# Kernel optimization log

Measured on AMD Instinct MI355X. Metric: run time of the kernel, lower is better.

Reference implementation:

```python
import jax, jax.numpy as jnp
import numpy as np

DIM = 192
NUM_HEADS = 6
WH, WW = 7, 7
N = WH * WW  # 49 tokens per window
C2 = 2 * DIM  # concatenated channel dim = 384
SCALE = (DIM // NUM_HEADS) ** -0.5  # module uses dim//num_heads, not C2//num_heads
NW = 64  # number of windows per image
B_ = 2048  # num_windows * batch


def _relative_position_index():
    ch = np.arange(WH)
    cw = np.arange(WW)
    coords = np.stack(np.meshgrid(ch, cw, indexing='ij')).reshape(2, -1)  # [2, N]
    rel = coords[:, :, None] - coords[:, None, :]  # [2, N, N]
    rel = rel.transpose(1, 2, 0).astype(np.int64)  # [N, N, 2]
    rel[..., 0] += WH - 1
    rel[..., 1] += WW - 1
    rel[..., 0] *= 2 * WW - 1
    return jnp.asarray(rel.sum(-1))  # [N, N]

REL_IDX = _relative_position_index()


def setup_inputs() -> dict:
    key = jax.random.key(0)
    ks = jax.random.split(key, 8)
    x = jax.random.normal(ks[0], (B_, N, DIM), dtype=jnp.float32)
    y = jax.random.normal(ks[1], (B_, N, DIM), dtype=jnp.float32)
    mask = jax.random.normal(ks[2], (NW, N, N), dtype=jnp.float32)
    w_qkv = jax.random.normal(ks[3], (6 * DIM, C2), dtype=jnp.float32) * 0.02
    b_qkv = jnp.zeros((6 * DIM,), dtype=jnp.float32)
    w_proj = jax.random.normal(ks[4], (DIM, C2), dtype=jnp.float32) * 0.02
    b_proj = jnp.zeros((DIM,), dtype=jnp.float32)
    bias_table = jax.random.normal(ks[5], ((2 * WH - 1) * (2 * WW - 1), NUM_HEADS), dtype=jnp.float32) * 0.02
    return {"x": x, "y": y, "mask": mask, "w_qkv": w_qkv, "b_qkv": b_qkv,
            "w_proj": w_proj, "b_proj": b_proj, "bias_table": bias_table}


def reference(x, y, mask, w_qkv, b_qkv, w_proj, b_proj, bias_table):
    Bc = x.shape[0]
    Dh = C2 // NUM_HEADS  # 64
    xy = jnp.concatenate([x, y], axis=2)  # [B_, N, 2*dim]
    qkv = xy @ w_qkv.T + b_qkv  # [B_, N, 6*dim]
    qkv = qkv.reshape(Bc, N, 3, NUM_HEADS, Dh).transpose(2, 0, 3, 1, 4)  # [3, B_, H, N, Dh]
    q, k, v = qkv[0] * SCALE, qkv[1], qkv[2]
    attn = jnp.einsum('bhnd,bhmd->bhnm', q, k)  # [B_, H, N, N]
    rpb = bias_table[REL_IDX]  # [N, N, H]
    attn = attn + rpb.transpose(2, 0, 1)[None]
    nW = mask.shape[0]
    attn = attn.reshape(Bc // nW, nW, NUM_HEADS, N, N) + mask[None, :, None]
    attn = attn.reshape(Bc, NUM_HEADS, N, N)
    attn = jax.nn.softmax(attn, axis=-1)
    out = jnp.einsum('bhnm,bhmd->bhnd', attn, v)  # [B_, H, N, Dh]
    out = out.transpose(0, 2, 1, 3).reshape(Bc, N, C2)
    return out @ w_proj.T + b_proj  # [B_, N, dim]
```

## Files before the change

### kernel.cpp

```cpp
#include <hip/hip_runtime.h>
#include <hip/hip_bf16.h>


typedef __attribute__((ext_vector_type(8))) short short8;
typedef __attribute__((ext_vector_type(4))) float f32x4;

#define SCALE 0.17677669529663687f

#define WQF_OFF    0ul
#define WQF_BYTES  (864ul*1024)
#define WPF_OFF    (WQF_OFF + WQF_BYTES)
#define WPF_BYTES  (144ul*1024)
#define COMB_OFF   (WPF_OFF + WPF_BYTES)
#define COMB_BYTES (64ul*6*4096*4)
#define WS_NEED    (COMB_OFF + COMB_BYTES)

__device__ __forceinline__ unsigned short f2bf(float f){
  unsigned u = __builtin_bit_cast(unsigned, f);
  u = u + 0x7fffu + ((u >> 16) & 1u);
  return (unsigned short)(u >> 16);
}
__device__ __forceinline__ unsigned long long pack4(float4 v){
  return (unsigned long long)f2bf(v.x) | ((unsigned long long)f2bf(v.y) << 16)
       | ((unsigned long long)f2bf(v.z) << 32) | ((unsigned long long)f2bf(v.w) << 48);
}

__device__ __forceinline__ unsigned short cvt1(float x){
  unsigned r;
  asm("v_cvt_pk_bf16_f32 %0, %1, %1" : "=v"(r) : "v"(x));
  return (unsigned short)r;
}
__device__ __forceinline__ uint2 pk4(float a, float b, float c, float d){
  unsigned lo, hi;
  asm("v_cvt_pk_bf16_f32 %0, %1, %2" : "=v"(lo) : "v"(a), "v"(b));
  asm("v_cvt_pk_bf16_f32 %0, %1, %2" : "=v"(hi) : "v"(c), "v"(d));
  return make_uint2(lo, hi);
}

__global__ void k_prep(const float* __restrict__ wq_f, const float* __restrict__ wp_f,
                       const float* __restrict__ mask, const float* __restrict__ btab,
                       unsigned short* __restrict__ wqf, unsigned short* __restrict__ wpf,
                       float* __restrict__ comb){
  if (blockIdx.x < 252){
    int t = blockIdx.x*256 + threadIdx.x;
    int fragidx = t >> 6, l = t & 63;
    const float* src; unsigned short* dst;
    float sc = 1.0f;
    if (fragidx < 864){
      int h = fragidx/144, rem = fragidx - h*144;
      int ct = rem/12, kt = rem - ct*12;
      int row = (ct>>2)*384 + h*64 + (ct&3)*16 + (l&15);
      src = wq_f + (long)row*384 + kt*32 + (l>>4)*8;
      dst = wqf + (long)fragidx*512 + l*8;
      if (ct < 4) sc = SCALE;
    } else {
      int fid = fragidx - 864;
      int ct = fid/12, kt = fid - ct*12;
      int row = ct*16 + (l&15);
      src = wp_f + (long)row*384 + kt*32 + (l>>4)*8;
      dst = wpf + (long)fid*512 + l*8;
    }
    short8 v;
    #pragma unroll
    for (int e = 0; e < 8; ++e) v[e] = (short)f2bf(src[e] * sc);
    *(short8*)dst = v;
  } else {
    int idx = (blockIdx.x - 252)*256 + threadIdx.x;
    int j = idx & 63, i = (idx >> 6) & 63, rest = idx >> 12;
    int h = rest % 6, w = rest / 6;
    float v;
    if (i < 49 && j < 49){
      int di = i / 7 - j / 7 + 6;
      int dj = i % 7 - j % 7 + 6;
      v = btab[(di * 13 + dj) * 6 + h] + mask[(w * 49 + i) * 49 + j];
    } else {
      v = (j >= 49) ? -1e30f : 0.0f;
    }
    comb[idx] = v;
  }
}

__device__ __forceinline__ int swz(int r, int b){ return b ^ ((r & 7) << 4); }
__device__ __forceinline__ int a_q (int r, int c){ return 49152 + swz(r, r*128 + c*2); }
__device__ __forceinline__ int a_k (int r, int c){ return 57344 + swz(r, r*128 + c*2); }
__device__ __forceinline__ int a_vt(int r, int c){ return 65536 + swz(r, r*128 + c*2); }
#define OBUF 73728

__global__ __launch_bounds__(256, 2)
void k_fused(const float* __restrict__ x, const float* __restrict__ y,
             const unsigned short* __restrict__ wqf, const unsigned short* __restrict__ wpf,
             const float* __restrict__ bqkv, const float* __restrict__ bproj,
             const float* __restrict__ comb, float* __restrict__ out){
  __shared__ __align__(16) unsigned char smem[81920];
  const int win = blockIdx.x;
  const int tid = threadIdx.x, w = tid>>6, l = tid&63, l15 = l&15, lg = l>>4;

  #pragma unroll
  for (int i = 0; i < 12; ++i){
    int f  = w*12 + i;
    int kt = f >> 2, mt = f & 3;
    int row = mt*16 + l15;
    int c   = kt*32 + lg*8;
    uint4 vv = make_uint4(0,0,0,0);
    if (row < 49){
      const float* src = (c < 192) ? (x + ((long)win*49 + row)*192 + c)
                                   : (y + ((long)win*49 + row)*192 + (c - 192));
      float4 f0 = *(const float4*)src, f1 = *(const float4*)(src + 4);
      uint2 lo = pk4(f0.x, f0.y, f0.z, f0.w);
      uint2 hi = pk4(f1.x, f1.y, f1.z, f1.w);
      vv = make_uint4(lo.x, lo.y, hi.x, hi.y);
    }
    *(uint4*)(smem + f*1024 + l*16) = vv;
  }

  int np[3];
  f32x4 pacc[4][3];
  #pragma unroll
  for (int nt = 0; nt < 3; ++nt){
    np[nt] = w*48 + nt*16 + l15;
    float bv = bproj[np[nt]];
    #pragma unroll
    for (int mt = 0; mt < 4; ++mt)
      #pragma unroll
      for (int j = 0; j < 4; ++j) pacc[mt][nt][j] = bv;
  }

  __syncthreads();

  #pragma unroll 2
  for (int h = 0; h < 6; ++h){
    const float* cb = comb + ((long)((win & 63)*6 + h))*4096 + (w*16 + l15)*64 + lg*4;
    float4 cbv[4];
    #pragma unroll
    for (int nt = 0; nt < 4; ++nt) cbv[nt] = *(const float4*)(cb + nt*16);

    float bias[3];
    #pragma unroll
    for (int nt = 0; nt < 3; ++nt){
      int ct = w*3 + nt, s = ct >> 2;
      bias[nt] = bqkv[s*384 + h*64 + (ct & 3)*16 + l15];
      if (s == 0) bias[nt] *= SCALE;
    }

    const unsigned short* Bb = wqf + ((long)h*12 + w*3)*12*512;
    short8 bB[2][3];
    #pragma unroll
    for (int nt = 0; nt < 3; ++nt)
      bB[0][nt] = *(const short8*)(Bb + (nt*12)*512 + l*8);
    f32x4 acc[4][3];
    #pragma unroll
    for (int mt = 0; mt < 4; ++mt)
      #pragma unroll
      for (int nt = 0; nt < 3; ++nt)
        #pragma unroll
        for (int j = 0; j < 4; ++j) acc[mt][nt][j] = bias[nt];

    #pragma unroll
    for (int kt = 0; kt < 12; ++kt){
      const int cur = kt & 1, nxt = cur ^ 1;
      if (kt < 11){
        #pragma unroll
        for (int nt = 0; nt < 3; ++nt)
          bB[nxt][nt] = *(const short8*)(Bb + (nt*12 + kt+1)*512 + l*8);
      }
      short8 aA[4];
      #pragma unroll
      for (int mt = 0; mt < 4; ++mt)
        aA[mt] = *(const short8*)(smem + (kt*4 + mt)*1024 + l*16);
      __builtin_amdgcn_s_setprio(1);
      #pragma unroll
      for (int nt = 0; nt < 3; ++nt){
        #pragma unroll
        for (int mt = 0; mt < 4; ++mt)
          acc[mt][nt] = __builtin_amdgcn_mfma_f32_16x16x32_bf16(aA[mt], bB[cur][nt], acc[mt][nt], 0, 0, 0);
      }
      __builtin_amdgcn_s_setprio(0);
    }

    #pragma unroll
    for (int nt = 0; nt < 3; ++nt){
      int ct = w*3 + nt, s = ct >> 2, d16 = (ct & 3) * 16;
      if (s == 2){
        #pragma unroll
        for (int mt = 0; mt < 4; ++mt){
          uint2 p = pk4(acc[mt][nt][0], acc[mt][nt][1], acc[mt][nt][2], acc[mt][nt][3]);
          *(uint2*)(smem + a_vt(d16 + l15, mt*16 + lg*4)) = p;
        }
      } else {
        #pragma unroll
        for (int mt = 0; mt < 4; ++mt){
          #pragma unroll
          for (int j = 0; j < 4; ++j){
            int row = mt*16 + lg*4 + j;
            int addr = (s == 0) ? a_q(row, d16 + l15) : a_k(row, d16 + l15);
            *(unsigned short*)(smem + addr) = cvt1(acc[mt][nt][j]);
          }
        }
      }
    }
    __syncthreads();

    short8 bq[2];
    #pragma unroll
    for (int ks = 0; ks < 2; ++ks)
      bq[ks] = *(const short8*)(smem + a_q(w*16 + l15, ks*32 + lg*8));
    f32x4 st[4] = {};
    __builtin_amdgcn_s_setprio(1);
    #pragma unroll
    for (int ks = 0; ks < 2; ++ks){
      #pragma unroll
      for (int nt = 0; nt < 4; ++nt){
        short8 ak = *(const short8*)(smem + a_k(nt*16 + l15, ks*32 + lg*8));
        st[nt] = __builtin_amdgcn_mfma_f32_16x16x32_bf16(ak, bq[ks], st[nt], 0, 0, 0);
      }
    }
    __builtin_amdgcn_s_setprio(0);
    #pragma unroll
    for (int nt = 0; nt < 4; ++nt){
      st[nt][0] += cbv[nt].x; st[nt][1] += cbv[nt].y;
      st[nt][2] += cbv[nt].z; st[nt][3] += cbv[nt].w;
    }
    float mx;
    {
      float m0 = fmaxf(fmaxf(st[0][0], st[0][1]), fmaxf(st[0][2], st[0][3]));
      float m1 = fmaxf(fmaxf(st[1][0], st[1][1]), fmaxf(st[1][2], st[1][3]));
      float m2 = fmaxf(fmaxf(st[2][0], st[2][1]), fmaxf(st[2][2], st[2][3]));
      float m3 = fmaxf(fmaxf(st[3][0], st[3][1]), fmaxf(st[3][2], st[3][3]));
      mx = fmaxf(fmaxf(m0, m1), fmaxf(m2, m3));
    }
    mx = fmaxf(mx, __shfl_xor(mx, 16));
    mx = fmaxf(mx, __shfl_xor(mx, 32));
    float ssum = 0.f;
    #pragma unroll
    for (int nt = 0; nt < 4; ++nt){
      #pragma unroll
      for (int j = 0; j < 4; ++j){
        float e = __expf(st[nt][j] - mx);
        st[nt][j] = e; ssum += e;
      }
    }
    ssum += __shfl_xor(ssum, 16);
    ssum += __shfl_xor(ssum, 32);
    const float inv = 1.0f / ssum;

    #pragma unroll
    for (int nt = 0; nt < 4; ++nt){
      uint2 p = pk4(st[nt][0]*inv, st[nt][1]*inv, st[nt][2]*inv, st[nt][3]*inv);
      *(uint2*)(smem + a_q(w*16 + l15, nt*16 + lg*4)) = p;
    }

    short8 ap[2];
    #pragma unroll
    for (int ks = 0; ks < 2; ++ks)
      ap[ks] = *(const short8*)(smem + a_q(w*16 + l15, ks*32 + lg*8));
    f32x4 oacc[4] = {};
    __builtin_amdgcn_s_setprio(1);
    #pragma unroll
    for (int ks = 0; ks < 2; ++ks){
      #pragma unroll
      for (int nt = 0; nt < 4; ++nt){
        short8 bv = *(const short8*)(smem + a_vt(nt*16 + l15, ks*32 + lg*8));
        oacc[nt] = __builtin_amdgcn_mfma_f32_16x16x32_bf16(ap[ks], bv, oacc[nt], 0, 0, 0);
      }
    }
    __builtin_amdgcn_s_setprio(0);

    short8 pb[2][3];
    #pragma unroll
    for (int ks = 0; ks < 2; ++ks)
      #pragma unroll
      for (int nt = 0; nt < 3; ++nt)
        pb[ks][nt] = *(const short8*)(wpf + ((long)(w*3 + nt)*12 + h*2 + ks)*512 + l*8);

    #pragma unroll
    for (int nt = 0; nt < 4; ++nt){
      int frag  = (nt >> 1)*4 + w;
      int chunk0 = (lg*4) + ((nt & 1)*2 + (l15 >> 3))*16;
      #pragma unroll
      for (int j = 0; j < 4; ++j){
        int addr = OBUF + frag*1024 + (chunk0 + j)*16 + (l15 & 7)*2;
        *(unsigned short*)(smem + addr) = cvt1(oacc[nt][j]);
      }
    }
    __syncthreads();

    #pragma unroll
    for (int ks = 0; ks < 2; ++ks){
      short8 aO[4];
      #pragma unroll
      for (int mt = 0; mt < 4; ++mt)
        aO[mt] = *(const short8*)(smem + OBUF + (ks*4 + mt)*1024 + l*16);
      __builtin_amdgcn_s_setprio(1);
      #pragma unroll
      for (int nt = 0; nt < 3; ++nt){
        #pragma unroll
        for (int mt = 0; mt < 4; ++mt)
          pacc[mt][nt] = __builtin_amdgcn_mfma_f32_16x16x32_bf16(aO[mt], pb[ks][nt], pacc[mt][nt], 0, 0, 0);
      }
      __builtin_amdgcn_s_setprio(0);
    }
  }

  #pragma unroll
  for (int mt = 0; mt < 4; ++mt){
    #pragma unroll
    for (int j = 0; j < 4; ++j){
      int row = mt*16 + lg*4 + j;
      if (row < 49){
        float* o = out + ((long)win*49 + row)*192;
        #pragma unroll
        for (int nt = 0; nt < 3; ++nt)
          o[np[nt]] = pacc[mt][nt][j];
      }
    }
  }
}

#define FB_WQ_ELEMS (1152*384)
#define FB_WP_ELEMS (192*384)
#define FB_WP_OFF   (FB_WQ_ELEMS*2)
#define FB_COMB_OFF (FB_WP_OFF + FB_WP_ELEMS*2)

__global__ void prep_weights_fb(const float* __restrict__ wq_f, const float* __restrict__ wp_f,
                                unsigned short* __restrict__ wq, unsigned short* __restrict__ wp){
  int gid = blockIdx.x * 256 + threadIdx.x;
  if (gid < FB_WQ_ELEMS) wq[gid] = f2bf(wq_f[gid]);
  else { int g = gid - FB_WQ_ELEMS; if (g < FB_WP_ELEMS) wp[g] = f2bf(wp_f[g]); }
}
__global__ void prep_comb_fb(const float* __restrict__ mask, const float* __restrict__ btab,
                             float* __restrict__ comb){
  int idx = blockIdx.x * 256 + threadIdx.x;
  int j = idx & 63, i = (idx >> 6) & 63, rest = idx >> 12;
  int h = rest % 6, w = rest / 6;
  float v;
  if (i < 49 && j < 49){
    int di = i / 7 - j / 7 + 6;
    int dj = i % 7 - j % 7 + 6;
    v = btab[(di * 13 + dj) * 6 + h] + mask[(w * 49 + i) * 49 + j];
  } else {
    v = (j >= 49) ? -1e30f : 0.0f;
  }
  comb[idx] = v;
}
__device__ __forceinline__ int fb_xy(int r, int c){ return 0      + swz(r, r*768 + c*2); }
__device__ __forceinline__ int fb_q (int r, int c){ return 49152  + swz(r, r*128 + c*2); }
__device__ __forceinline__ int fb_k (int r, int c){ return 57344  + swz(r, r*128 + c*2); }
__device__ __forceinline__ int fb_vt(int r, int c){ return 65536  + swz(r, r*128 + c*2); }
__device__ __forceinline__ int fb_p (int r, int c){ return 73728  + swz(r, r*128 + c*2); }

__global__ __launch_bounds__(256, 2)
void fused_attn_fb(const float* __restrict__ x, const float* __restrict__ y,
                   const float* __restrict__ bqkv, const float* __restrict__ bproj,
                   const unsigned short* __restrict__ wq, const unsigned short* __restrict__ wp,
                   const float* __restrict__ comb, float* __restrict__ out){
  __shared__ __align__(16) unsigned char smem[81920];
  const int b = blockIdx.x, tid = threadIdx.x;
  const int w = tid>>6, l = tid&63, l15 = l&15, lg = l>>4;
  {
    const float4* x4 = (const float4*)x + b * 2352;
    const float4* y4 = (const float4*)y + b * 2352;
    for (int idx = tid; idx < 2352; idx += 256){
      int r = idx / 48, c4 = (idx % 48) * 4;
      float4 vx = x4[idx], vy = y4[idx];
      *(unsigned long long*)(smem + fb_xy(r, c4))       = pack4(vx);
      *(unsigned long long*)(smem + fb_xy(r, 192 + c4)) = pack4(vy);
    }
    for (int idx = tid; idx < 1440; idx += 256){
      int r = 49 + idx / 96, c4 = (idx % 96) * 4;
      *(unsigned long long*)(smem + fb_xy(r, c4)) = 0ull;
    }
  }
  __syncthreads();
  const float* cbB = comb + (long)(b & 63) * (6 * 4096);
  f32x4 pacc[4][3] = {};
  int np[3]; float bp[3];
  #pragma unroll
  for (int nt = 0; nt < 3; ++nt){ np[nt] = w*48 + nt*16 + l15; bp[nt] = bproj[np[nt]]; }
  #pragma unroll 1
  for (int h = 0; h < 6; ++h){
    f32x4 acc[4][3] = {};
    int wrow[3]; float bias[3];
    #pragma unroll
    for (int nt = 0; nt < 3; ++nt){
      int n = np[nt];
      wrow[nt] = (n >> 6) * 384 + h * 64 + (n & 63);
      bias[nt] = bqkv[wrow[nt]];
    }
    #pragma unroll 4
    for (int kt = 0; kt < 12; ++kt){
      int k0 = kt * 32;
      short8 a[4];
      #pragma unroll
      for (int mt = 0; mt < 4; ++mt)
        a[mt] = *(const short8*)(smem + fb_xy(mt*16 + l15, k0 + lg*8));
      #pragma unroll
      for (int nt = 0; nt < 3; ++nt){
        short8 bb = *(const short8*)(wq + (long)wrow[nt]*384 + k0 + lg*8);
        #pragma unroll
        for (int mt = 0; mt < 4; ++mt)
          acc[mt][nt] = __builtin_amdgcn_mfma_f32_16x16x32_bf16(a[mt], bb, acc[mt][nt], 0, 0, 0);
      }
    }
    #pragma unroll
    for (int nt = 0; nt < 3; ++nt){
      int n = np[nt], s = n >> 6, d = n & 63;
      #pragma unroll
      for (int mt = 0; mt < 4; ++mt){
        #pragma unroll
        for (int j = 0; j < 4; ++j){
          int row = mt*16 + lg*4 + j;
          float v = acc[mt][nt][j] + bias[nt];
          if (s == 0) v *= SCALE;
          int addr = (s==0) ? fb_q(row,d) : (s==1) ? fb_k(row,d) : fb_vt(d,row);
          *(unsigned short*)(smem + addr) = f2bf(v);
        }
      }
    }
    __syncthreads();
    short8 aq[2];
    #pragma unroll
    for (int ks = 0; ks < 2; ++ks)
      aq[ks] = *(const short8*)(smem + fb_q(w*16 + l15, ks*32 + lg*8));
    f32x4 sacc[4] = {};
    #pragma unroll
    for (int ks = 0; ks < 2; ++ks)
      #pragma unroll
      for (int nt = 0; nt < 4; ++nt){
        short8 bk = *(const short8*)(smem + fb_k(nt*16 + l15, ks*32 + lg*8));
        sacc[nt] = __builtin_amdgcn_mfma_f32_16x16x32_bf16(aq[ks], bk, sacc[nt], 0, 0, 0);
      }
    const float* cb = cbB + h * 4096;
    float rs[4];
    #pragma unroll
    for (int j = 0; j < 4; ++j){
      int r = w*16 + lg*4 + j;
      #pragma unroll
      for (int nt = 0; nt < 4; ++nt) sacc[nt][j] += cb[r*64 + nt*16 + l15];
      float m = fmaxf(fmaxf(sacc[0][j], sacc[1][j]), fmaxf(sacc[2][j], sacc[3][j]));
      #pragma unroll
      for (int dlt = 1; dlt < 16; dlt <<= 1) m = fmaxf(m, __shfl_xor(m, dlt));
      float ssum = 0.f;
      #pragma unroll
      for (int nt = 0; nt < 4; ++nt){
        float e = __expf(sacc[nt][j] - m);
        sacc[nt][j] = e; ssum += e;
      }
      #pragma unroll
      for (int dlt = 1; dlt < 16; dlt <<= 1) ssum += __shfl_xor(ssum, dlt);
      rs[j] = ssum;
      #pragma unroll
      for (int nt = 0; nt < 4; ++nt)
        *(unsigned short*)(smem + fb_p(r, nt*16 + l15)) = f2bf(sacc[nt][j]);
    }
    short8 ap[2];
    #pragma unroll
    for (int ks = 0; ks < 2; ++ks)
      ap[ks] = *(const short8*)(smem + fb_p(w*16 + l15, ks*32 + lg*8));
    f32x4 oacc[4] = {};
    #pragma unroll
    for (int ks = 0; ks < 2; ++ks)
      #pragma unroll
      for (int nt = 0; nt < 4; ++nt){
        short8 bv = *(const short8*)(smem + fb_vt(nt*16 + l15, ks*32 + lg*8));
        oacc[nt] = __builtin_amdgcn_mfma_f32_16x16x32_bf16(ap[ks], bv, oacc[nt], 0, 0, 0);
      }
    float inv[4];
    #pragma unroll
    for (int j = 0; j < 4; ++j) inv[j] = 1.0f / rs[j];
    #pragma unroll
    for (int nt = 0; nt < 4; ++nt)
      #pragma unroll
      for (int j = 0; j < 4; ++j){
        int row = w*16 + lg*4 + j;
        *(unsigned short*)(smem + fb_p(row, nt*16 + l15)) = f2bf(oacc[nt][j] * inv[j]);
      }
    __syncthreads();
    #pragma unroll
    for (int ks = 0; ks < 2; ++ks){
      short8 ao8[4];
      #pragma unroll
      for (int mt = 0; mt < 4; ++mt)
        ao8[mt] = *(const short8*)(smem + fb_p(mt*16 + l15, ks*32 + lg*8));
      #pragma unroll
      for (int nt = 0; nt < 3; ++nt){
        short8 bb = *(const short8*)(wp + (long)np[nt]*384 + h*64 + ks*32 + lg*8);
        #pragma unroll
        for (int mt = 0; mt < 4; ++mt)
          pacc[mt][nt] = __builtin_amdgcn_mfma_f32_16x16x32_bf16(ao8[mt], bb, pacc[mt][nt], 0, 0, 0);
      }
    }
  }
  #pragma unroll
  for (int mt = 0; mt < 4; ++mt)
    #pragma unroll
    for (int j = 0; j < 4; ++j){
      int row = mt*16 + lg*4 + j;
      if (row < 49){
        float* o = out + ((long)b*49 + row)*192;
        #pragma unroll
        for (int nt = 0; nt < 3; ++nt)
          o[np[nt]] = pacc[mt][nt][j] + bp[nt];
      }
    }
}

extern "C" void kernel_launch(void* const* d_in, const int* in_sizes, int n_in,
                              void* d_out, int out_size, void* d_ws, size_t ws_size,
                              hipStream_t stream){
  (void)in_sizes; (void)n_in; (void)out_size;
  const float* x     = (const float*)d_in[0];
  const float* y     = (const float*)d_in[1];
  const float* mask  = (const float*)d_in[2];
  const float* wq_f  = (const float*)d_in[3];
  const float* bqkv  = (const float*)d_in[4];
  const float* wp_f  = (const float*)d_in[5];
  const float* bproj = (const float*)d_in[6];
  const float* btab  = (const float*)d_in[7];
  float* out = (float*)d_out;

  if (ws_size >= WS_NEED){
    unsigned short* wqf = (unsigned short*)((char*)d_ws + WQF_OFF);
    unsigned short* wpf = (unsigned short*)((char*)d_ws + WPF_OFF);
    float*          cmb = (float*)((char*)d_ws + COMB_OFF);
    hipLaunchKernelGGL(k_prep,  dim3(6396), dim3(256), 0, stream,
                       wq_f, wp_f, mask, btab, wqf, wpf, cmb);
    hipLaunchKernelGGL(k_fused, dim3(2048), dim3(256), 0, stream,
                       x, y, wqf, wpf, bqkv, bproj, cmb, out);
  } else {
    unsigned short* wq  = (unsigned short*)d_ws;
    unsigned short* wp  = (unsigned short*)((char*)d_ws + FB_WP_OFF);
    float*          cmb = (float*)((char*)d_ws + FB_COMB_OFF);
    hipLaunchKernelGGL(prep_weights_fb, dim3(2016), dim3(256), 0, stream, wq_f, wp_f, wq, wp);
    hipLaunchKernelGGL(prep_comb_fb,    dim3(6144), dim3(256), 0, stream, mask, btab, cmb);
    hipLaunchKernelGGL(fused_attn_fb,   dim3(2048), dim3(256), 0, stream,
                       x, y, bqkv, bproj, wq, wp, cmb, out);
  }
}
```

Before: 270.7 us.

## Pre-convert x/y to bf16 fragments and double-buffer per-head LDS

Adds a separate kernel that converts x and y into bf16 MFMA fragment layout in workspace. The fused kernel now reads its A operands directly from global memory instead of staging them in LDS. Q/K/V LDS regions are double-buffered by head, which removes the second per-head barrier. The output-projection tile is kept per wave, with each wave computing its own 16 rows across all 192 output columns, so LDS shrinks and occupancy may rise. In exchange it adds an extra pass that writes and reads about 100MB of bf16 activations, and it re-reads A fragments from global for every head.

```diff
diff --git a/kernel.cpp b/kernel.cpp
--- a/kernel.cpp
+++ b/kernel.cpp
@@ -13,7 +13,9 @@
 #define WPF_BYTES  (144ul*1024)
 #define COMB_OFF   (WPF_OFF + WPF_BYTES)
 #define COMB_BYTES (64ul*6*4096*4)
-#define WS_NEED    (COMB_OFF + COMB_BYTES)
+#define XYF_OFF    (COMB_OFF + COMB_BYTES)
+#define XYF_BYTES  (2048ul*48*1024)
+#define WS_NEED    (XYF_OFF + XYF_BYTES)
 
 __device__ __forceinline__ unsigned short f2bf(float f){
   unsigned u = __builtin_bit_cast(unsigned, f);
@@ -80,55 +82,55 @@
   }
 }
 
+__global__ void k1_xyfrag(const float* __restrict__ x, const float* __restrict__ y,
+                          unsigned short* __restrict__ xyf){
+  const int kt  = blockIdx.x;
+  const int win = blockIdx.y;
+  const int mt  = threadIdx.x >> 6;
+  const int l   = threadIdx.x & 63;
+  const int row = mt*16 + (l & 15);
+  const int c0  = kt*32 + (l >> 4)*8;
+  short8 v = {};
+  if (row < 49){
+    const float* src = (kt < 6) ? (x + ((long)win*49 + row)*192 + c0)
+                                : (y + ((long)win*49 + row)*192 + (c0 - 192));
+    float4 f0 = *(const float4*)src, f1 = *(const float4*)(src+4);
+    unsigned long long lo = pack4(f0), hi = pack4(f1);
+    #pragma unroll
+    for (int e = 0; e < 4; ++e){ v[e] = (short)(lo >> (16*e)); v[4+e] = (short)(hi >> (16*e)); }
+  }
+  *(short8*)(xyf + (((long)win*12 + kt)*4 + mt)*512 + l*8) = v;
+}
+
 __device__ __forceinline__ int swz(int r, int b){ return b ^ ((r & 7) << 4); }
-__device__ __forceinline__ int a_q (int r, int c){ return 49152 + swz(r, r*128 + c*2); }
-__device__ __forceinline__ int a_k (int r, int c){ return 57344 + swz(r, r*128 + c*2); }
-__device__ __forceinline__ int a_vt(int r, int c){ return 65536 + swz(r, r*128 + c*2); }
-#define OBUF 73728
+__device__ __forceinline__ int a_q (int b, int r, int c){ return b*24576 +         swz(r, r*128 + c*2); }
+__device__ __forceinline__ int a_k (int b, int r, int c){ return b*24576 + 8192  + swz(r, r*128 + c*2); }
+__device__ __forceinline__ int a_vt(int b, int r, int c){ return b*24576 + 16384 + swz(r, r*128 + c*2); }
+__device__ __forceinline__ int a_o (int w, int r, int c){ return 49152 + w*2048 + swz(r, r*128 + c*2); }
 
 __global__ __launch_bounds__(256, 2)
-void k_fused(const float* __restrict__ x, const float* __restrict__ y,
+void k_fused(const unsigned short* __restrict__ xyf,
              const unsigned short* __restrict__ wqf, const unsigned short* __restrict__ wpf,
              const float* __restrict__ bqkv, const float* __restrict__ bproj,
              const float* __restrict__ comb, float* __restrict__ out){
-  __shared__ __align__(16) unsigned char smem[81920];
+  __shared__ __align__(16) unsigned char smem[57344];
   const int win = blockIdx.x;
   const int tid = threadIdx.x, w = tid>>6, l = tid&63, l15 = l&15, lg = l>>4;
 
+  f32x4 pacc[12];
   #pragma unroll
-  for (int i = 0; i < 12; ++i){
-    int f  = w*12 + i;
-    int kt = f >> 2, mt = f & 3;
-    int row = mt*16 + l15;
-    int c   = kt*32 + lg*8;
-    uint4 vv = make_uint4(0,0,0,0);
-    if (row < 49){
-      const float* src = (c < 192) ? (x + ((long)win*49 + row)*192 + c)
-                                   : (y + ((long)win*49 + row)*192 + (c - 192));
-      float4 f0 = *(const float4*)src, f1 = *(const float4*)(src + 4);
-      uint2 lo = pk4(f0.x, f0.y, f0.z, f0.w);
-      uint2 hi = pk4(f1.x, f1.y, f1.z, f1.w);
-      vv = make_uint4(lo.x, lo.y, hi.x, hi.y);
-    }
-    *(uint4*)(smem + f*1024 + l*16) = vv;
-  }
-
-  int np[3];
-  f32x4 pacc[4][3];
-  #pragma unroll
-  for (int nt = 0; nt < 3; ++nt){
-    np[nt] = w*48 + nt*16 + l15;
-    float bv = bproj[np[nt]];
-    #pragma unroll
-    for (int mt = 0; mt < 4; ++mt)
-      #pragma unroll
-      for (int j = 0; j < 4; ++j) pacc[mt][nt][j] = bv;
-  }
-
-  __syncthreads();
-
-  #pragma unroll 2
+  for (int nt2 = 0; nt2 < 12; ++nt2){
+    float bv = bproj[nt2*16 + l15];
+    #pragma unroll
+    for (int j = 0; j < 4; ++j) pacc[nt2][j] = bv;
+  }
+
+  const unsigned short* Ab = xyf + (long)win*24576;
+
+  #pragma unroll 1
   for (int h = 0; h < 6; ++h){
+    const int cur = h & 1;
+
     const float* cb = comb + ((long)((win & 63)*6 + h))*4096 + (w*16 + l15)*64 + lg*4;
     float4 cbv[4];
     #pragma unroll
@@ -157,22 +159,22 @@
 
     #pragma unroll
     for (int kt = 0; kt < 12; ++kt){
-      const int cur = kt & 1, nxt = cur ^ 1;
+      const int curb = kt & 1, nxtb = curb ^ 1;
       if (kt < 11){
         #pragma unroll
         for (int nt = 0; nt < 3; ++nt)
-          bB[nxt][nt] = *(const short8*)(Bb + (nt*12 + kt+1)*512 + l*8);
+          bB[nxtb][nt] = *(const short8*)(Bb + (nt*12 + kt+1)*512 + l*8);
       }
       short8 aA[4];
       #pragma unroll
       for (int mt = 0; mt < 4; ++mt)
-        aA[mt] = *(const short8*)(smem + (kt*4 + mt)*1024 + l*16);
+        aA[mt] = *(const short8*)(Ab + (kt*4 + mt)*512 + l*8);
       __builtin_amdgcn_s_setprio(1);
       #pragma unroll
       for (int nt = 0; nt < 3; ++nt){
         #pragma unroll
         for (int mt = 0; mt < 4; ++mt)
-          acc[mt][nt] = __builtin_amdgcn_mfma_f32_16x16x32_bf16(aA[mt], bB[cur][nt], acc[mt][nt], 0, 0, 0);
+          acc[mt][nt] = __builtin_amdgcn_mfma_f32_16x16x32_bf16(aA[mt], bB[curb][nt], acc[mt][nt], 0, 0, 0);
       }
       __builtin_amdgcn_s_setprio(0);
     }
@@ -184,7 +186,7 @@
         #pragma unroll
         for (int mt = 0; mt < 4; ++mt){
           uint2 p = pk4(acc[mt][nt][0], acc[mt][nt][1], acc[mt][nt][2], acc[mt][nt][3]);
-          *(uint2*)(smem + a_vt(d16 + l15, mt*16 + lg*4)) = p;
+          *(uint2*)(smem + a_vt(cur, d16 + l15, mt*16 + lg*4)) = p;
         }
       } else {
         #pragma unroll
@@ -192,7 +194,7 @@
           #pragma unroll
           for (int j = 0; j < 4; ++j){
             int row = mt*16 + lg*4 + j;
-            int addr = (s == 0) ? a_q(row, d16 + l15) : a_k(row, d16 + l15);
+            int addr = (s == 0) ? a_q(cur, row, d16 + l15) : a_k(cur, row, d16 + l15);
             *(unsigned short*)(smem + addr) = cvt1(acc[mt][nt][j]);
           }
         }
@@ -203,14 +205,14 @@
     short8 bq[2];
     #pragma unroll
     for (int ks = 0; ks < 2; ++ks)
-      bq[ks] = *(const short8*)(smem + a_q(w*16 + l15, ks*32 + lg*8));
+      bq[ks] = *(const short8*)(smem + a_q(cur, w*16 + l15, ks*32 + lg*8));
     f32x4 st[4] = {};
     __builtin_amdgcn_s_setprio(1);
     #pragma unroll
     for (int ks = 0; ks < 2; ++ks){
       #pragma unroll
       for (int nt = 0; nt < 4; ++nt){
-        short8 ak = *(const short8*)(smem + a_k(nt*16 + l15, ks*32 + lg*8));
+        short8 ak = *(const short8*)(smem + a_k(cur, nt*16 + l15, ks*32 + lg*8));
         st[nt] = __builtin_amdgcn_mfma_f32_16x16x32_bf16(ak, bq[ks], st[nt], 0, 0, 0);
       }
     }
@@ -246,72 +248,52 @@
     #pragma unroll
     for (int nt = 0; nt < 4; ++nt){
       uint2 p = pk4(st[nt][0]*inv, st[nt][1]*inv, st[nt][2]*inv, st[nt][3]*inv);
-      *(uint2*)(smem + a_q(w*16 + l15, nt*16 + lg*4)) = p;
+      *(uint2*)(smem + a_q(cur, w*16 + l15, nt*16 + lg*4)) = p;
     }
 
     short8 ap[2];
     #pragma unroll
     for (int ks = 0; ks < 2; ++ks)
-      ap[ks] = *(const short8*)(smem + a_q(w*16 + l15, ks*32 + lg*8));
+      ap[ks] = *(const short8*)(smem + a_q(cur, w*16 + l15, ks*32 + lg*8));
     f32x4 oacc[4] = {};
     __builtin_amdgcn_s_setprio(1);
     #pragma unroll
     for (int ks = 0; ks < 2; ++ks){
       #pragma unroll
       for (int nt = 0; nt < 4; ++nt){
-        short8 bv = *(const short8*)(smem + a_vt(nt*16 + l15, ks*32 + lg*8));
+        short8 bv = *(const short8*)(smem + a_vt(cur, nt*16 + l15, ks*32 + lg*8));
         oacc[nt] = __builtin_amdgcn_mfma_f32_16x16x32_bf16(ap[ks], bv, oacc[nt], 0, 0, 0);
       }
     }
     __builtin_amdgcn_s_setprio(0);
 
-    short8 pb[2][3];
-    #pragma unroll
-    for (int ks = 0; ks < 2; ++ks)
-      #pragma unroll
-      for (int nt = 0; nt < 3; ++nt)
-        pb[ks][nt] = *(const short8*)(wpf + ((long)(w*3 + nt)*12 + h*2 + ks)*512 + l*8);
-
-    #pragma unroll
-    for (int nt = 0; nt < 4; ++nt){
-      int frag  = (nt >> 1)*4 + w;
-      int chunk0 = (lg*4) + ((nt & 1)*2 + (l15 >> 3))*16;
-      #pragma unroll
-      for (int j = 0; j < 4; ++j){
-        int addr = OBUF + frag*1024 + (chunk0 + j)*16 + (l15 & 7)*2;
-        *(unsigned short*)(smem + addr) = cvt1(oacc[nt][j]);
-      }
-    }
-    __syncthreads();
+    #pragma unroll
+    for (int nt = 0; nt < 4; ++nt)
+      #pragma unroll
+      for (int j = 0; j < 4; ++j)
+        *(unsigned short*)(smem + a_o(w, lg*4 + j, nt*16 + l15)) = cvt1(oacc[nt][j]);
 
     #pragma unroll
     for (int ks = 0; ks < 2; ++ks){
-      short8 aO[4];
-      #pragma unroll
-      for (int mt = 0; mt < 4; ++mt)
-        aO[mt] = *(const short8*)(smem + OBUF + (ks*4 + mt)*1024 + l*16);
+      short8 aO = *(const short8*)(smem + a_o(w, l15, ks*32 + lg*8));
       __builtin_amdgcn_s_setprio(1);
       #pragma unroll
-      for (int nt = 0; nt < 3; ++nt){
-        #pragma unroll
-        for (int mt = 0; mt < 4; ++mt)
-          pacc[mt][nt] = __builtin_amdgcn_mfma_f32_16x16x32_bf16(aO[mt], pb[ks][nt], pacc[mt][nt], 0, 0, 0);
+      for (int nt2 = 0; nt2 < 12; ++nt2){
+        short8 bb = *(const short8*)(wpf + ((long)nt2*12 + h*2 + ks)*512 + l*8);
+        pacc[nt2] = __builtin_amdgcn_mfma_f32_16x16x32_bf16(aO, bb, pacc[nt2], 0, 0, 0);
       }
       __builtin_amdgcn_s_setprio(0);
     }
   }
 
   #pragma unroll
-  for (int mt = 0; mt < 4; ++mt){
-    #pragma unroll
-    for (int j = 0; j < 4; ++j){
-      int row = mt*16 + lg*4 + j;
-      if (row < 49){
-        float* o = out + ((long)win*49 + row)*192;
-        #pragma unroll
-        for (int nt = 0; nt < 3; ++nt)
-          o[np[nt]] = pacc[mt][nt][j];
-      }
+  for (int j = 0; j < 4; ++j){
+    int row = w*16 + lg*4 + j;
+    if (row < 49){
+      float* o = out + ((long)win*49 + row)*192;
+      #pragma unroll
+      for (int nt2 = 0; nt2 < 12; ++nt2)
+        o[nt2*16 + l15] = pacc[nt2][j];
     }
   }
 }
@@ -522,10 +504,12 @@
     unsigned short* wqf = (unsigned short*)((char*)d_ws + WQF_OFF);
     unsigned short* wpf = (unsigned short*)((char*)d_ws + WPF_OFF);
     float*          cmb = (float*)((char*)d_ws + COMB_OFF);
-    hipLaunchKernelGGL(k_prep,  dim3(6396), dim3(256), 0, stream,
+    unsigned short* xyf = (unsigned short*)((char*)d_ws + XYF_OFF);
+    hipLaunchKernelGGL(k_prep,    dim3(6396),    dim3(256), 0, stream,
                        wq_f, wp_f, mask, btab, wqf, wpf, cmb);
-    hipLaunchKernelGGL(k_fused, dim3(2048), dim3(256), 0, stream,
-                       x, y, wqf, wpf, bqkv, bproj, cmb, out);
+    hipLaunchKernelGGL(k1_xyfrag, dim3(12,2048), dim3(256), 0, stream, x, y, xyf);
+    hipLaunchKernelGGL(k_fused,   dim3(2048),    dim3(256), 0, stream,
+                       xyf, wqf, wpf, bqkv, bproj, cmb, out);
   } else {
     unsigned short* wq  = (unsigned short*)d_ws;
     unsigned short* wp  = (unsigned short*)((char*)d_ws + FB_WP_OFF);
```

After: 1.033 ms. 282% more time.
